# Kernel optimization log

Measured on AMD Instinct MI355X. Metric: run time of the kernel, lower is better.

## Reference

```python
import jax, jax.numpy as jnp
import numpy as np


def _he_scale(k, shape, fan_in):
    return jax.random.normal(k, shape, dtype=jnp.float32) * np.sqrt(2.0 / fan_in).astype(np.float32)


def setup_inputs() -> dict:
    key = jax.random.key(0)
    kx, kt, kp, kg, kf = jax.random.split(key, 5)
    B, H, W, C, D = 4, 64, 64, 256, 128
    x = jax.random.normal(kx, (B, H, W, C), dtype=jnp.float32)
    Wt = _he_scale(kt, (C, D), C)
    Wp = _he_scale(kp, (C, D), C)
    Wg = _he_scale(kg, (C, D), C)
    Wf = _he_scale(kf, (D, C), D)
    return {"x": x, "Wt": Wt, "Wp": Wp, "Wg": Wg, "Wf": Wf}


def _maxpool1d(z, pool_size=2, stride=1):
    # Keras MaxPool1D, padding='valid': output length = (N - pool_size)//stride + 1
    return jax.lax.reduce_window(
        z, -jnp.inf, jax.lax.max,
        window_dimensions=(1, pool_size, 1),
        window_strides=(1, stride, 1),
        padding='VALID')


def reference(x, Wt, Wp, Wg, Wf):
    B, H, W, C = x.shape
    D = Wt.shape[1]
    N = H * W
    # 1x1 conv projections == per-position matmuls
    theta = jnp.einsum('bhwc,cd->bhwd', x, Wt).reshape(B, N, D)   # [B,N,D]
    phi = jnp.einsum('bhwc,cd->bhwd', x, Wp).reshape(B, N, D)     # [B,N,D]
    g = jnp.einsum('bhwc,cd->bhwd', x, Wg).reshape(B, N, D)       # [B,N,D]
    # embedded mode: subsample phi and g (pool_size=2, strides=1) -> M = N-1
    phi = _maxpool1d(phi)                                          # [B,M,D]
    g = _maxpool1d(g)                                              # [B,M,D]
    # f = theta @ phi^T, softmax over keys (no scaling in embedded mode)
    f = jax.nn.softmax(jnp.einsum('bnd,bmd->bnm', theta, phi), axis=-1)  # [B,N,M]
    y = jnp.einsum('bnm,bmd->bnd', f, g).reshape(B, H, W, D)       # [B,H,W,D]
    # final 1x1 conv back to C channels + residual
    z = x + jnp.einsum('bhwd,dc->bhwc', y, Wf)
    return z
```

## Files before the change

### kernel.cpp

```cpp
#include <hip/hip_runtime.h>

#define B_  4
#define N_  4096
#define C_  256
#define D_  128
#define M_  4095
#define BN_ (B_ * N_)

typedef _Float16 half_t;
typedef __attribute__((ext_vector_type(8))) _Float16 half8;
typedef __attribute__((ext_vector_type(4))) _Float16 half4;
typedef __attribute__((ext_vector_type(4))) float f32x4;

#define MFMA16x16x32(A, B, C) __builtin_amdgcn_mfma_f32_16x16x32_f16(A, B, C, 0, 0, 0)
#define LOG2E 1.44269504088896f
#define RTHR  5.0f

#define SWZ(r, c) ((c) ^ (((r) & 7) << 3))

__global__ __launch_bounds__(256) void prep_kernel(
    const float* __restrict__ Wt, const float* __restrict__ Wp,
    const float* __restrict__ Wg, const float* __restrict__ Wf,
    half_t* __restrict__ WT_hi, half_t* __restrict__ WfT)
{
    const int idx = blockIdx.x * 256 + threadIdx.x;
    const int wsel = blockIdx.y;
    if (wsel < 3) {
        const float* __restrict__ W = (wsel == 0) ? Wt : (wsel == 1) ? Wp : Wg;
        const int d = idx >> 8, c = idx & 255;
        WT_hi[(size_t)wsel * 32768 + idx] = (half_t)W[(size_t)c * D_ + d];
    } else {
        const int c = idx >> 7, d = idx & 127;
        WfT[idx] = (half_t)Wf[(size_t)d * C_ + c];
    }
}

__global__ __launch_bounds__(256) void proj_kernel(
    const float* __restrict__ x, const half_t* __restrict__ WT_hi,
    half_t* __restrict__ theta, half_t* __restrict__ pphi,
    half_t* __restrict__ pgT)
{
    const int tid = threadIdx.x;
    const int lane = tid & 63;
    const int w = tid >> 6;
    const int lm = lane & 15;
    const int lq = lane >> 4;
    const int r0 = blockIdx.x * 64;
    const int which = blockIdx.y;
    const half_t* __restrict__ Wg_ = WT_hi + (size_t)which * 32768;

    __shared__ __align__(16) unsigned char lds_raw[30720];
    half_t (*Xh)[64][40]   = (half_t (*)[64][40])(lds_raw);
    half_t (*Whl)[128][40] = (half_t (*)[128][40])(lds_raw + 10240);

    f32x4 acc[8];
#pragma unroll
    for (int nb = 0; nb < 8; ++nb)
#pragma unroll
        for (int r = 0; r < 4; ++r) acc[nb][r] = 0.f;

    const int xr = tid >> 2, xc = (tid & 3) * 8;
    const int wr = tid >> 1, wc = (tid & 1) * 16;

    const float* xs = x + (size_t)(r0 + xr) * C_ + xc;
    const half_t* wsrc = Wg_ + (size_t)wr * 256 + wc;
    float4 xv0 = *(const float4*)&xs[0];
    float4 xv1 = *(const float4*)&xs[4];
    half8 wv0 = *(const half8*)&wsrc[0];
    half8 wv1 = *(const half8*)&wsrc[8];
    {
        half8 hi;
        hi[0] = (half_t)xv0.x; hi[1] = (half_t)xv0.y;
        hi[2] = (half_t)xv0.z; hi[3] = (half_t)xv0.w;
        hi[4] = (half_t)xv1.x; hi[5] = (half_t)xv1.y;
        hi[6] = (half_t)xv1.z; hi[7] = (half_t)xv1.w;
        *(half8*)&Xh[0][xr][xc] = hi;
        *(half8*)&Whl[0][wr][wc]     = wv0;
        *(half8*)&Whl[0][wr][wc + 8] = wv1;
    }

    int cur = 0;
    for (int kc = 0; kc < 8; ++kc) {
        if (kc < 7) {
            xs += 32; wsrc += 32;
            xv0 = *(const float4*)&xs[0];
            xv1 = *(const float4*)&xs[4];
            wv0 = *(const half8*)&wsrc[0];
            wv1 = *(const half8*)&wsrc[8];
        }
        __syncthreads();

        half8 ah = *(const half8*)&Xh[cur][w * 16 + lm][lq * 8];
#pragma unroll
        for (int nb = 0; nb < 8; ++nb) {
            half8 bh = *(const half8*)&Whl[cur][nb * 16 + lm][lq * 8];
            acc[nb] = MFMA16x16x32(ah, bh, acc[nb]);
        }

        if (kc < 7) {
            half8 hi;
            hi[0] = (half_t)xv0.x; hi[1] = (half_t)xv0.y;
            hi[2] = (half_t)xv0.z; hi[3] = (half_t)xv0.w;
            hi[4] = (half_t)xv1.x; hi[5] = (half_t)xv1.y;
            hi[6] = (half_t)xv1.z; hi[7] = (half_t)xv1.w;
            *(half8*)&Xh[cur ^ 1][xr][xc] = hi;
            *(half8*)&Whl[cur ^ 1][wr][wc]     = wv0;
            *(half8*)&Whl[cur ^ 1][wr][wc + 8] = wv1;
            cur ^= 1;
        }
    }

    if (which == 0) {
#pragma unroll
        for (int nb = 0; nb < 8; ++nb)
#pragma unroll
            for (int r = 0; r < 4; ++r)
                theta[(size_t)(r0 + w * 16 + lq * 4 + r) * D_ + nb * 16 + lm] =
                    (half_t)(acc[nb][r] * LOG2E);
        return;
    }

    __syncthreads();
    half_t (*LsT)[72] = (half_t (*)[72])(lds_raw);
#pragma unroll
    for (int nb = 0; nb < 8; ++nb) {
        const int d = nb * 16 + lm;
        const int m = w * 16 + lq * 4;
        half4 pk;
#pragma unroll
        for (int r = 0; r < 4; ++r) pk[r] = (half_t)acc[nb][r];
        *(half4*)&LsT[d][m] = pk;
    }
    if (tid < 128) {
        int rh = r0 + 64;
        if ((rh & (N_ - 1)) == 0) rh = r0 + 63;
        const float* xrow = x + (size_t)rh * C_;
        const half_t* wrow = Wg_ + (size_t)tid * 256;
        float s = 0.f;
#pragma unroll
        for (int c8 = 0; c8 < 32; ++c8) {
            half8 h = *(const half8*)&wrow[c8 * 8];
            float4 xa = *(const float4*)&xrow[c8 * 8];
            float4 xb = *(const float4*)&xrow[c8 * 8 + 4];
            s += xa.x * (float)h[0] + xa.y * (float)h[1]
               + xa.z * (float)h[2] + xa.w * (float)h[3]
               + xb.x * (float)h[4] + xb.y * (float)h[5]
               + xb.z * (float)h[6] + xb.w * (float)h[7];
        }
        LsT[tid][64] = (half_t)s;
    }
    __syncthreads();

    if (which == 1) {
        const int m = tid >> 2, dh = (tid & 3) * 32;
        half8 o[4];
#pragma unroll
        for (int j = 0; j < 32; ++j) {
            float v0 = (float)LsT[dh + j][m];
            float v1 = (float)LsT[dh + j][m + 1];
            o[j >> 3][j & 7] = (half_t)fmaxf(v0, v1);
        }
        half8* dst = (half8*)&pphi[(size_t)(r0 + m) * D_ + dh];
#pragma unroll
        for (int j = 0; j < 4; ++j) dst[j] = o[j];
    } else {
        const int d = tid >> 1, mh = (tid & 1) * 32;
        const int b = r0 / N_, m0 = r0 & (N_ - 1);
        half8 in[4];
#pragma unroll
        for (int j = 0; j < 4; ++j) in[j] = *(const half8*)&LsT[d][mh + j * 8];
        const half_t ext = LsT[d][mh + 32];
        half8 o[4];
#pragma unroll
        for (int j = 0; j < 32; ++j) {
            float v0 = (float)in[j >> 3][j & 7];
            float v1 = (j == 31) ? (float)ext : (float)in[(j + 1) >> 3][(j + 1) & 7];
            o[j >> 3][j & 7] = (half_t)fmaxf(v0, v1);
        }
        half8* dst = (half8*)&pgT[((size_t)b * D_ + d) * N_ + m0 + mh];
#pragma unroll
        for (int j = 0; j < 4; ++j) dst[j] = o[j];
    }
}

template<int KS>
__global__ __launch_bounds__(256, 2) void attn_kernel(
    const half_t* __restrict__ theta, const half_t* __restrict__ pphi,
    const half_t* __restrict__ pgT, half_t* __restrict__ ypart,
    float* __restrict__ mstat, float* __restrict__ lstat)
{
    const int TILES = 64 / KS;
    const int tid = threadIdx.x;
    const int lane = tid & 63;
    const int w = tid >> 6;
    const int lm = lane & 15;
    const int lq = lane >> 4;
    const int qt = blockIdx.x, ksb = blockIdx.y, b = blockIdx.z;
    const int q0 = qt * 128;
    const int kt0 = ksb * TILES, kt1 = kt0 + TILES;

    __shared__ half_t Ks[64][136];
    __shared__ half_t Gts[128][72];
    __shared__ half_t Ps[128][72];

    half8 qh[2][4];
#pragma unroll
    for (int nb = 0; nb < 2; ++nb) {
        const half_t* tr_ = theta + ((size_t)b * N_ + q0 + w * 32 + nb * 16 + lm) * D_;
#pragma unroll
        for (int k4 = 0; k4 < 4; ++k4)
            qh[nb][k4] = *(const half8*)(tr_ + k4 * 32 + lq * 8);
    }

    const int key = tid >> 2, ch = tid & 3;
    const int gdd = tid >> 1, gkh = tid & 1;
    const float4* ksrc = (const float4*)(pphi +
        ((size_t)b * N_ + kt0 * 64 + key) * D_ + ch * 32);
    const float4* gsrc = (const float4*)(pgT +
        ((size_t)b * D_ + gdd) * N_ + kt0 * 64 + gkh * 32);

    float m_i[2] = {-1e30f, -1e30f};
    float l_i[2] = {0.f, 0.f};
    f32x4 yacc[2][8];
#pragma unroll
    for (int mb = 0; mb < 2; ++mb)
#pragma unroll
        for (int dn = 0; dn < 8; ++dn)
#pragma unroll
            for (int r = 0; r < 4; ++r) yacc[mb][dn][r] = 0.f;

    for (int kt = kt0; kt < kt1; ++kt) {
        const int k0 = kt * 64;
        __syncthreads();
        {
            float4 a0 = ksrc[0], a1 = ksrc[1], a2 = ksrc[2], a3 = ksrc[3];
            float4 g0 = gsrc[0], g1 = gsrc[1], g2 = gsrc[2], g3 = gsrc[3];
            ksrc += 1024;
            gsrc += 8;
            float4* kdst = (float4*)&Ks[key][ch * 32];
            kdst[0] = a0; kdst[1] = a1; kdst[2] = a2; kdst[3] = a3;
            float4* gdst = (float4*)&Gts[gdd][gkh * 32];
            gdst[0] = g0; gdst[1] = g1; gdst[2] = g2; gdst[3] = g3;
        }
        __syncthreads();

        f32x4 sc[4][2];
#pragma unroll
        for (int kb = 0; kb < 4; ++kb)
#pragma unroll
            for (int nb = 0; nb < 2; ++nb)
#pragma unroll
                for (int r = 0; r < 4; ++r) sc[kb][nb][r] = 0.f;
        __builtin_amdgcn_s_setprio(1);
#pragma unroll
        for (int kb = 0; kb < 4; ++kb) {
#pragma unroll
            for (int k4 = 0; k4 < 4; ++k4) {
                half8 kf = *(const half8*)&Ks[kb * 16 + lm][k4 * 32 + lq * 8];
#pragma unroll
                for (int nb = 0; nb < 2; ++nb)
                    sc[kb][nb] = MFMA16x16x32(kf, qh[nb][k4], sc[kb][nb]);
            }
        }
        __builtin_amdgcn_s_setprio(0);
        if (k0 + 64 > M_) {
#pragma unroll
            for (int kb = 0; kb < 4; ++kb)
#pragma unroll
                for (int r = 0; r < 4; ++r)
                    if (k0 + kb * 16 + lq * 4 + r >= M_) {
                        sc[kb][0][r] = -1e30f; sc[kb][1][r] = -1e30f;
                    }
        }

        float mt[2];
#pragma unroll
        for (int nb = 0; nb < 2; ++nb) {
            float m0 = -1e30f;
#pragma unroll
            for (int kb = 0; kb < 4; ++kb)
#pragma unroll
                for (int r = 0; r < 4; ++r) m0 = fmaxf(m0, sc[kb][nb][r]);
            m0 = fmaxf(m0, __shfl_xor(m0, 16, 64));
            m0 = fmaxf(m0, __shfl_xor(m0, 32, 64));
            mt[nb] = m0;
        }
        const bool need0 = __any(mt[0] > m_i[0] + RTHR);
        const bool need1 = __any(mt[1] > m_i[1] + RTHR);
        float alphav[2] = {1.f, 1.f};
#pragma unroll
        for (int nb = 0; nb < 2; ++nb) {
            const bool need = nb ? need1 : need0;
            float mnew = m_i[nb];
            if (need) {
                mnew = fmaxf(m_i[nb], mt[nb]);
                alphav[nb] = exp2f(m_i[nb] - mnew);
                m_i[nb] = mnew;
            }
            float rs = 0.f;
#pragma unroll
            for (int kb = 0; kb < 4; ++kb) {
                half4 pk;
#pragma unroll
                for (int r = 0; r < 4; ++r) {
                    float p = exp2f(sc[kb][nb][r] - mnew);
                    rs += p;
                    pk[r] = (half_t)p;
                }
                *(half4*)&Ps[w * 32 + nb * 16 + lm][kb * 16 + lq * 4] = pk;
            }
            l_i[nb] = l_i[nb] * alphav[nb] + rs;
        }
        if (need0) {
            float a_t[4];
#pragma unroll
            for (int r = 0; r < 4; ++r) a_t[r] = __shfl(alphav[0], lq * 4 + r, 16);
#pragma unroll
            for (int dn = 0; dn < 8; ++dn)
#pragma unroll
                for (int r = 0; r < 4; ++r) yacc[0][dn][r] *= a_t[r];
        }
        if (need1) {
            float a_t[4];
#pragma unroll
            for (int r = 0; r < 4; ++r) a_t[r] = __shfl(alphav[1], lq * 4 + r, 16);
#pragma unroll
            for (int dn = 0; dn < 8; ++dn)
#pragma unroll
                for (int r = 0; r < 4; ++r) yacc[1][dn][r] *= a_t[r];
        }

        half8 pf[2][2];
#pragma unroll
        for (int mb = 0; mb < 2; ++mb)
#pragma unroll
            for (int k2 = 0; k2 < 2; ++k2)
                pf[mb][k2] = *(const half8*)&Ps[w * 32 + mb * 16 + lm][k2 * 32 + lq * 8];
        __builtin_amdgcn_s_setprio(1);
#pragma unroll
        for (int dn = 0; dn < 8; ++dn) {
#pragma unroll
            for (int k2 = 0; k2 < 2; ++k2) {
                half8 gf = *(const half8*)&Gts[dn * 16 + lm][k2 * 32 + lq * 8];
                yacc[0][dn] = MFMA16x16x32(pf[0][k2], gf, yacc[0][dn]);
                yacc[1][dn] = MFMA16x16x32(pf[1][k2], gf, yacc[1][dn]);
            }
        }
        __builtin_amdgcn_s_setprio(0);
    }

#pragma unroll
    for (int nb = 0; nb < 2; ++nb) {
        l_i[nb] += __shfl_xor(l_i[nb], 16, 64);
        l_i[nb] += __shfl_xor(l_i[nb], 32, 64);
    }
    half_t* yp = ypart + ((size_t)ksb * BN_ + (size_t)b * N_) * D_;
#pragma unroll
    for (int mb = 0; mb < 2; ++mb)
#pragma unroll
        for (int dn = 0; dn < 8; ++dn)
#pragma unroll
            for (int r = 0; r < 4; ++r)
                yp[(size_t)(q0 + w * 32 + mb * 16 + lq * 4 + r) * D_ + dn * 16 + lm] =
                    (half_t)yacc[mb][dn][r];
    if (lq == 0) {
#pragma unroll
        for (int nb = 0; nb < 2; ++nb) {
            const int row = q0 + w * 32 + nb * 16 + lm;
            mstat[(size_t)ksb * BN_ + (size_t)b * N_ + row] = m_i[nb];
            lstat[(size_t)ksb * BN_ + (size_t)b * N_ + row] = l_i[nb];
        }
    }
}

template<int KS>
__global__ __launch_bounds__(256) void merge_kernel(
    const half_t* __restrict__ ypart, const float* __restrict__ mstat,
    const float* __restrict__ lstat, half_t* __restrict__ ymerged)
{
    const int idx = blockIdx.x * 256 + threadIdx.x;
    const int row = idx >> 4;
    const int c8 = (idx & 15) * 8;

    float mv[KS], lv[KS], wv[KS];
    float Mx = -1e30f;
#pragma unroll
    for (int s = 0; s < KS; ++s) {
        mv[s] = mstat[(size_t)s * BN_ + row];
        lv[s] = lstat[(size_t)s * BN_ + row];
        Mx = fmaxf(Mx, mv[s]);
    }
    float lsum = 0.f;
#pragma unroll
    for (int s = 0; s < KS; ++s) { wv[s] = exp2f(mv[s] - Mx); lsum += wv[s] * lv[s]; }
    const float inv = 1.f / lsum;
#pragma unroll
    for (int s = 0; s < KS; ++s) wv[s] *= inv;

    const size_t yb = (size_t)row * D_ + c8;
    float m[8];
#pragma unroll
    for (int j = 0; j < 8; ++j) m[j] = 0.f;
#pragma unroll
    for (int s = 0; s < KS; ++s) {
        half8 yv = *(const half8*)&ypart[(size_t)s * BN_ * D_ + yb];
#pragma unroll
        for (int j = 0; j < 8; ++j) m[j] += wv[s] * (float)yv[j];
    }
    half8 o;
#pragma unroll
    for (int j = 0; j < 8; ++j) o[j] = (half_t)m[j];
    *(half8*)&ymerged[yb] = o;
}

__global__ __launch_bounds__(256) void final_kernel(
    const half_t* __restrict__ ymerged, const float* __restrict__ x,
    const half_t* __restrict__ WfT, float* __restrict__ out)
{
    const int tid = threadIdx.x;
    const int lane = tid & 63;
    const int w = tid >> 6;
    const int lm = lane & 15;
    const int lq = lane >> 4;
    const int r0 = blockIdx.x * 64;
    const int c0 = blockIdx.y * 128;

    __shared__ half_t Ys[64][128];
    __shared__ half_t Wfs[128][128];

    {
        const int wc = tid >> 1, wd = (tid & 1) * 64;
        const half_t* wf = WfT + (size_t)(c0 + wc) * D_ + wd;
#pragma unroll
        for (int q = 0; q < 8; ++q)
            *(half8*)&Wfs[wc][SWZ(wc, wd + q * 8)] = *(const half8*)&wf[q * 8];
    }
    {
        const int sr = tid >> 2;
        const int dd = (tid & 3) * 32;
        const half_t* ym = ymerged + (size_t)(r0 + sr) * D_ + dd;
#pragma unroll
        for (int q = 0; q < 4; ++q)
            *(half8*)&Ys[sr][SWZ(sr, dd + q * 8)] = *(const half8*)&ym[q * 8];
    }
    __syncthreads();

    f32x4 acc[8];
#pragma unroll
    for (int nb = 0; nb < 8; ++nb)
#pragma unroll
        for (int r = 0; r < 4; ++r) acc[nb][r] = 0.f;

    const int yrow = w * 16 + lm;
#pragma unroll
    for (int k4 = 0; k4 < 4; ++k4) {
        half8 af = *(const half8*)&Ys[yrow][SWZ(yrow, k4 * 32 + lq * 8)];
#pragma unroll
        for (int nb = 0; nb < 8; ++nb) {
            const int wrow = nb * 16 + lm;
            half8 bf = *(const half8*)&Wfs[wrow][SWZ(wrow, k4 * 32 + lq * 8)];
            acc[nb] = MFMA16x16x32(af, bf, acc[nb]);
        }
    }

#pragma unroll
    for (int nb = 0; nb < 8; ++nb)
#pragma unroll
        for (int r = 0; r < 4; ++r) {
            const int row = r0 + w * 16 + lq * 4 + r;
            const int col = c0 + nb * 16 + lm;
            out[(size_t)row * C_ + col] =
                acc[nb][r] + x[(size_t)row * C_ + col];
        }
}

extern "C" void kernel_launch(void* const* d_in, const int* in_sizes, int n_in,
                              void* d_out, int out_size, void* d_ws, size_t ws_size,
                              hipStream_t stream)
{
    const float* x  = (const float*)d_in[0];
    const float* Wt = (const float*)d_in[1];
    const float* Wp = (const float*)d_in[2];
    const float* Wg = (const float*)d_in[3];
    const float* Wf = (const float*)d_in[4];
    float* out = (float*)d_out;

    const size_t SEG = (size_t)BN_ * D_;

    const size_t need8 = (size_t)(3 + 8 + 1) * SEG * 2
                       + (size_t)2 * 8 * BN_ * 4 + 131072 * 2;
    const int KS = (ws_size >= need8) ? 8 : 4;

    half_t* hb      = (half_t*)d_ws;
    half_t* theta   = hb;
    half_t* pphi    = hb + SEG;
    half_t* pgT     = hb + 2 * SEG;
    half_t* ypart   = hb + 3 * SEG;
    half_t* ymerged = hb + (size_t)(3 + KS) * SEG;
    float*  mstat   = (float*)(hb + (size_t)(3 + KS + 1) * SEG);
    float*  lstat   = mstat + (size_t)KS * BN_;
    half_t* WT_hi   = (half_t*)(lstat + (size_t)KS * BN_);
    half_t* WfT     = WT_hi + 3 * 32768;

    prep_kernel<<<dim3(128, 4), 256, 0, stream>>>(Wt, Wp, Wg, Wf, WT_hi, WfT);
    proj_kernel<<<dim3(BN_ / 64, 3), 256, 0, stream>>>(x, WT_hi, theta, pphi, pgT);
    if (KS == 8) {
        attn_kernel<8><<<dim3(N_ / 128, 8, B_), 256, 0, stream>>>(
            theta, pphi, pgT, ypart, mstat, lstat);
        merge_kernel<8><<<dim3(BN_ * 16 / 256), 256, 0, stream>>>(
            ypart, mstat, lstat, ymerged);
    } else {
        attn_kernel<4><<<dim3(N_ / 128, 4, B_), 256, 0, stream>>>(
            theta, pphi, pgT, ypart, mstat, lstat);
        merge_kernel<4><<<dim3(BN_ * 16 / 256), 256, 0, stream>>>(
            ypart, mstat, lstat, ymerged);
    }
    final_kernel<<<dim3(BN_ / 64, 2), 256, 0, stream>>>(ymerged, x, WfT, out);
}
```

Before: 165.6 us.

## Double query rows per attention block to reuse K/G tiles across more queries

Each attention block now processes 256 queries instead of 128, and each wave handles 64 query rows in two pairs of 16-row groups. This halves the number of K/G tile loads into shared memory per query and raises the MFMA work per synchronization. The cost is more accumulator and query registers, a larger P buffer in shared memory, and half as many blocks in the grid, which risks spills or lower occupancy.

```diff
diff --git a/kernel.cpp b/kernel.cpp
--- a/kernel.cpp
+++ b/kernel.cpp
@@ -196,17 +196,17 @@
     const int lm = lane & 15;
     const int lq = lane >> 4;
     const int qt = blockIdx.x, ksb = blockIdx.y, b = blockIdx.z;
-    const int q0 = qt * 128;
+    const int q0 = qt * 256;
     const int kt0 = ksb * TILES, kt1 = kt0 + TILES;
 
     __shared__ half_t Ks[64][136];
     __shared__ half_t Gts[128][72];
-    __shared__ half_t Ps[128][72];
-
-    half8 qh[2][4];
-#pragma unroll
-    for (int nb = 0; nb < 2; ++nb) {
-        const half_t* tr_ = theta + ((size_t)b * N_ + q0 + w * 32 + nb * 16 + lm) * D_;
+    __shared__ half_t Ps[256][72];
+
+    half8 qh[4][4];
+#pragma unroll
+    for (int nb = 0; nb < 4; ++nb) {
+        const half_t* tr_ = theta + ((size_t)b * N_ + q0 + w * 64 + nb * 16 + lm) * D_;
 #pragma unroll
         for (int k4 = 0; k4 < 4; ++k4)
             qh[nb][k4] = *(const half8*)(tr_ + k4 * 32 + lq * 8);
@@ -219,11 +219,11 @@
     const float4* gsrc = (const float4*)(pgT +
         ((size_t)b * D_ + gdd) * N_ + kt0 * 64 + gkh * 32);
 
-    float m_i[2] = {-1e30f, -1e30f};
-    float l_i[2] = {0.f, 0.f};
-    f32x4 yacc[2][8];
-#pragma unroll
-    for (int mb = 0; mb < 2; ++mb)
+    float m_i[4] = {-1e30f, -1e30f, -1e30f, -1e30f};
+    float l_i[4] = {0.f, 0.f, 0.f, 0.f};
+    f32x4 yacc[4][8];
+#pragma unroll
+    for (int mb = 0; mb < 4; ++mb)
 #pragma unroll
         for (int dn = 0; dn < 8; ++dn)
 #pragma unroll
@@ -244,129 +244,126 @@
         }
         __syncthreads();
 
-        f32x4 sc[4][2];
-#pragma unroll
-        for (int kb = 0; kb < 4; ++kb)
-#pragma unroll
-            for (int nb = 0; nb < 2; ++nb)
-#pragma unroll
-                for (int r = 0; r < 4; ++r) sc[kb][nb][r] = 0.f;
-        __builtin_amdgcn_s_setprio(1);
-#pragma unroll
-        for (int kb = 0; kb < 4; ++kb) {
-#pragma unroll
-            for (int k4 = 0; k4 < 4; ++k4) {
-                half8 kf = *(const half8*)&Ks[kb * 16 + lm][k4 * 32 + lq * 8];
-#pragma unroll
-                for (int nb = 0; nb < 2; ++nb)
-                    sc[kb][nb] = MFMA16x16x32(kf, qh[nb][k4], sc[kb][nb]);
+        bool need[4];
+        float alphav[4];
+#pragma unroll
+        for (int pr = 0; pr < 2; ++pr) {
+            const int nbA = pr * 2, nbB = pr * 2 + 1;
+            f32x4 sc[4][2];
+#pragma unroll
+            for (int kb = 0; kb < 4; ++kb)
+#pragma unroll
+                for (int u = 0; u < 2; ++u)
+#pragma unroll
+                    for (int r = 0; r < 4; ++r) sc[kb][u][r] = 0.f;
+            __builtin_amdgcn_s_setprio(1);
+#pragma unroll
+            for (int kb = 0; kb < 4; ++kb) {
+#pragma unroll
+                for (int k4 = 0; k4 < 4; ++k4) {
+                    half8 kf = *(const half8*)&Ks[kb * 16 + lm][k4 * 32 + lq * 8];
+                    sc[kb][0] = MFMA16x16x32(kf, qh[nbA][k4], sc[kb][0]);
+                    sc[kb][1] = MFMA16x16x32(kf, qh[nbB][k4], sc[kb][1]);
+                }
             }
-        }
-        __builtin_amdgcn_s_setprio(0);
-        if (k0 + 64 > M_) {
-#pragma unroll
-            for (int kb = 0; kb < 4; ++kb)
+            __builtin_amdgcn_s_setprio(0);
+            if (k0 + 64 > M_) {
+#pragma unroll
+                for (int kb = 0; kb < 4; ++kb)
+#pragma unroll
+                    for (int r = 0; r < 4; ++r)
+                        if (k0 + kb * 16 + lq * 4 + r >= M_) {
+                            sc[kb][0][r] = -1e30f; sc[kb][1][r] = -1e30f;
+                        }
+            }
+#pragma unroll
+            for (int u = 0; u < 2; ++u) {
+                const int nb = pr * 2 + u;
+                float m0 = -1e30f;
+#pragma unroll
+                for (int kb = 0; kb < 4; ++kb)
+#pragma unroll
+                    for (int r = 0; r < 4; ++r) m0 = fmaxf(m0, sc[kb][u][r]);
+                m0 = fmaxf(m0, __shfl_xor(m0, 16, 64));
+                m0 = fmaxf(m0, __shfl_xor(m0, 32, 64));
+                const bool nd = __any(m0 > m_i[nb] + RTHR);
+                need[nb] = nd;
+                float mnew = m_i[nb];
+                float av = 1.f;
+                if (nd) {
+                    mnew = fmaxf(m_i[nb], m0);
+                    av = exp2f(m_i[nb] - mnew);
+                    m_i[nb] = mnew;
+                }
+                alphav[nb] = av;
+                float rs = 0.f;
+                const int prow = w * 64 + nb * 16 + lm;
+#pragma unroll
+                for (int kb = 0; kb < 4; ++kb) {
+                    half4 pk;
+#pragma unroll
+                    for (int r = 0; r < 4; ++r) {
+                        float p = exp2f(sc[kb][u][r] - mnew);
+                        rs += p;
+                        pk[r] = (half_t)p;
+                    }
+                    *(half4*)&Ps[prow][kb * 16 + lq * 4] = pk;
+                }
+                l_i[nb] = l_i[nb] * av + rs;
+            }
+        }
+#pragma unroll
+        for (int nb = 0; nb < 4; ++nb) {
+            if (need[nb]) {
+                float a_t[4];
 #pragma unroll
                 for (int r = 0; r < 4; ++r)
-                    if (k0 + kb * 16 + lq * 4 + r >= M_) {
-                        sc[kb][0][r] = -1e30f; sc[kb][1][r] = -1e30f;
-                    }
-        }
-
-        float mt[2];
-#pragma unroll
-        for (int nb = 0; nb < 2; ++nb) {
-            float m0 = -1e30f;
-#pragma unroll
-            for (int kb = 0; kb < 4; ++kb)
-#pragma unroll
-                for (int r = 0; r < 4; ++r) m0 = fmaxf(m0, sc[kb][nb][r]);
-            m0 = fmaxf(m0, __shfl_xor(m0, 16, 64));
-            m0 = fmaxf(m0, __shfl_xor(m0, 32, 64));
-            mt[nb] = m0;
-        }
-        const bool need0 = __any(mt[0] > m_i[0] + RTHR);
-        const bool need1 = __any(mt[1] > m_i[1] + RTHR);
-        float alphav[2] = {1.f, 1.f};
-#pragma unroll
-        for (int nb = 0; nb < 2; ++nb) {
-            const bool need = nb ? need1 : need0;
-            float mnew = m_i[nb];
-            if (need) {
-                mnew = fmaxf(m_i[nb], mt[nb]);
-                alphav[nb] = exp2f(m_i[nb] - mnew);
-                m_i[nb] = mnew;
+                    a_t[r] = __shfl(alphav[nb], lq * 4 + r, 16);
+#pragma unroll
+                for (int dn = 0; dn < 8; ++dn)
+#pragma unroll
+                    for (int r = 0; r < 4; ++r) yacc[nb][dn][r] *= a_t[r];
             }
-            float rs = 0.f;
-#pragma unroll
-            for (int kb = 0; kb < 4; ++kb) {
-                half4 pk;
-#pragma unroll
-                for (int r = 0; r < 4; ++r) {
-                    float p = exp2f(sc[kb][nb][r] - mnew);
-                    rs += p;
-                    pk[r] = (half_t)p;
-                }
-                *(half4*)&Ps[w * 32 + nb * 16 + lm][kb * 16 + lq * 4] = pk;
-            }
-            l_i[nb] = l_i[nb] * alphav[nb] + rs;
-        }
-        if (need0) {
-            float a_t[4];
-#pragma unroll
-            for (int r = 0; r < 4; ++r) a_t[r] = __shfl(alphav[0], lq * 4 + r, 16);
-#pragma unroll
-            for (int dn = 0; dn < 8; ++dn)
-#pragma unroll
-                for (int r = 0; r < 4; ++r) yacc[0][dn][r] *= a_t[r];
-        }
-        if (need1) {
-            float a_t[4];
-#pragma unroll
-            for (int r = 0; r < 4; ++r) a_t[r] = __shfl(alphav[1], lq * 4 + r, 16);
-#pragma unroll
-            for (int dn = 0; dn < 8; ++dn)
-#pragma unroll
-                for (int r = 0; r < 4; ++r) yacc[1][dn][r] *= a_t[r];
-        }
-
-        half8 pf[2][2];
-#pragma unroll
-        for (int mb = 0; mb < 2; ++mb)
+        }
+
+        half8 pf[4][2];
+#pragma unroll
+        for (int mb = 0; mb < 4; ++mb)
 #pragma unroll
             for (int k2 = 0; k2 < 2; ++k2)
-                pf[mb][k2] = *(const half8*)&Ps[w * 32 + mb * 16 + lm][k2 * 32 + lq * 8];
+                pf[mb][k2] = *(const half8*)&Ps[w * 64 + mb * 16 + lm][k2 * 32 + lq * 8];
         __builtin_amdgcn_s_setprio(1);
 #pragma unroll
         for (int dn = 0; dn < 8; ++dn) {
 #pragma unroll
             for (int k2 = 0; k2 < 2; ++k2) {
                 half8 gf = *(const half8*)&Gts[dn * 16 + lm][k2 * 32 + lq * 8];
-                yacc[0][dn] = MFMA16x16x32(pf[0][k2], gf, yacc[0][dn]);
-                yacc[1][dn] = MFMA16x16x32(pf[1][k2], gf, yacc[1][dn]);
+#pragma unroll
+                for (int mb = 0; mb < 4; ++mb)
+                    yacc[mb][dn] = MFMA16x16x32(pf[mb][k2], gf, yacc[mb][dn]);
             }
         }
         __builtin_amdgcn_s_setprio(0);
     }
 
 #pragma unroll
-    for (int nb = 0; nb < 2; ++nb) {
+    for (int nb = 0; nb < 4; ++nb) {
         l_i[nb] += __shfl_xor(l_i[nb], 16, 64);
         l_i[nb] += __shfl_xor(l_i[nb], 32, 64);
     }
     half_t* yp = ypart + ((size_t)ksb * BN_ + (size_t)b * N_) * D_;
 #pragma unroll
-    for (int mb = 0; mb < 2; ++mb)
+    for (int mb = 0; mb < 4; ++mb)
 #pragma unroll
         for (int dn = 0; dn < 8; ++dn)
 #pragma unroll
             for (int r = 0; r < 4; ++r)
-                yp[(size_t)(q0 + w * 32 + mb * 16 + lq * 4 + r) * D_ + dn * 16 + lm] =
+                yp[(size_t)(q0 + w * 64 + mb * 16 + lq * 4 + r) * D_ + dn * 16 + lm] =
                     (half_t)yacc[mb][dn][r];
     if (lq == 0) {
 #pragma unroll
-        for (int nb = 0; nb < 2; ++nb) {
-            const int row = q0 + w * 32 + nb * 16 + lm;
+        for (int nb = 0; nb < 4; ++nb) {
+            const int row = q0 + w * 64 + nb * 16 + lm;
             mstat[(size_t)ksb * BN_ + (size_t)b * N_ + row] = m_i[nb];
             lstat[(size_t)ksb * BN_ + (size_t)b * N_ + row] = l_i[nb];
         }
@@ -505,12 +502,12 @@
     prep_kernel<<<dim3(128, 4), 256, 0, stream>>>(Wt, Wp, Wg, Wf, WT_hi, WfT);
     proj_kernel<<<dim3(BN_ / 64, 3), 256, 0, stream>>>(x, WT_hi, theta, pphi, pgT);
     if (KS == 8) {
-        attn_kernel<8><<<dim3(N_ / 128, 8, B_), 256, 0, stream>>>(
+        attn_kernel<8><<<dim3(N_ / 256, 8, B_), 256, 0, stream>>>(
             theta, pphi, pgT, ypart, mstat, lstat);
         merge_kernel<8><<<dim3(BN_ * 16 / 256), 256, 0, stream>>>(
             ypart, mstat, lstat, ymerged);
     } else {
-        attn_kernel<4><<<dim3(N_ / 128, 4, B_), 256, 0, stream>>>(
+        attn_kernel<4><<<dim3(N_ / 256, 4, B_), 256, 0, stream>>>(
             theta, pphi, pgT, ypart, mstat, lstat);
         merge_kernel<4><<<dim3(BN_ * 16 / 256), 256, 0, stream>>>(
             ypart, mstat, lstat, ymerged);
```

Result: slower. 199.6 us (+20.5%).
